# Kernel tuning notes

Hardware: AMD Instinct MI355X
Metric: run time of the kernel (lower is better)

Reference implementation:

```python
import jax, jax.numpy as jnp
import numpy as np

EMBED_DIM = 1024
NUM_HEADS = 16
HEAD_DIM = EMBED_DIM // NUM_HEADS


def setup_inputs() -> dict:
    key = jax.random.key(0)
    k_x, k_wqkv, k_bqkv, k_wo, k_bo = jax.random.split(key, 5)
    b, n = 2, 2048
    scale_in = 1.0 / np.sqrt(EMBED_DIM)
    return {
        "x": jax.random.normal(k_x, (b, n, EMBED_DIM), dtype=jnp.float32),
        "W_qkv": jax.random.normal(k_wqkv, (EMBED_DIM, 3 * EMBED_DIM), dtype=jnp.float32) * scale_in,
        "b_qkv": jnp.zeros((3 * EMBED_DIM,), dtype=jnp.float32),
        "W_out": jax.random.normal(k_wo, (EMBED_DIM, EMBED_DIM), dtype=jnp.float32) * scale_in,
        "b_out": jnp.zeros((EMBED_DIM,), dtype=jnp.float32),
    }


def _rope_rotate(t, cos, sin):
    # t: [b, h, n, hd]; cos/sin: [1, 1, n, hd//2]
    t1, t2 = jnp.split(t, 2, axis=-1)
    return jnp.concatenate([cos * t1 - sin * t2, sin * t1 + cos * t2], axis=-1)


def reference(x, W_qkv, b_qkv, W_out, b_out):
    b, n, d = x.shape
    h, hd = NUM_HEADS, HEAD_DIM

    qkv = x @ W_qkv + b_qkv                      # [b, n, 3d]
    q, k, v = jnp.split(qkv, 3, axis=-1)
    q, k, v = [t.reshape(b, n, h, hd).transpose(0, 2, 1, 3) for t in (q, k, v)]

    # RoPE tables
    hd2 = hd // 2
    theta = 10000.0 ** (-2.0 * jnp.arange(hd2, dtype=jnp.float32) / hd)
    freqs = jnp.arange(n, dtype=jnp.float32)[:, None] * theta[None, :]  # [n, hd2]
    cos = jnp.cos(freqs)[None, None]
    sin = jnp.sin(freqs)[None, None]
    q = _rope_rotate(q, cos, sin)
    k = _rope_rotate(k, cos, sin)

    scores = jnp.einsum('bhqd,bhkd->bhqk', q, k) / jnp.sqrt(jnp.float32(hd))
    attn = jax.nn.softmax(scores, axis=-1)       # [b, h, n, n]
    out = jnp.einsum('bhqk,bhkd->bhqd', attn, v)
    out = out.transpose(0, 2, 1, 3).reshape(b, n, d)
    return out @ W_out + b_out
```

## Files before the change

kernel.cpp:

```cpp
#include <hip/hip_runtime.h>
#include <hip/hip_bf16.h>
#include <math.h>

#define EMBED 1024
#define NHEAD 16
#define HD 64
#define BATCH 2
#define SEQ 2048
#define MTOT (BATCH * SEQ)
#define QKVN (3 * EMBED)

typedef __attribute__((ext_vector_type(8))) short short8;
typedef __attribute__((ext_vector_type(4))) float f32x4;

typedef __attribute__((address_space(1))) const unsigned int GUI;
typedef __attribute__((address_space(3))) unsigned int LUI;

__device__ __forceinline__ void gload_lds16(const void* src, void* dst) {
  __builtin_amdgcn_global_load_lds((GUI*)src, (LUI*)dst, 16, 0, 0);
}

__device__ __forceinline__ unsigned short f2bf(float f) {
  unsigned u = __builtin_bit_cast(unsigned, f);
  u += 0x7fffu + ((u >> 16) & 1u);
  return (unsigned short)(u >> 16);
}

__device__ __forceinline__ unsigned cvt_pk_bf16(float lo, float hi) {
  unsigned r;
  asm("v_cvt_pk_bf16_f32 %0, %1, %2" : "=v"(r) : "v"(lo), "v"(hi));
  return r;
}

#if __has_builtin(__builtin_amdgcn_exp2f)
#define EXP2(x) __builtin_amdgcn_exp2f(x)
#else
#define EXP2(x) __builtin_exp2f(x)
#endif

#define QSCALE 0.1803368801111191f


__global__ __launch_bounds__(256) void k_cvt(const float* __restrict__ in,
                                             unsigned short* __restrict__ out, int n4) {
  int i = blockIdx.x * 256 + threadIdx.x;
  if (i >= n4) return;
  float4 v = reinterpret_cast<const float4*>(in)[i];
  ushort4 o;
  o.x = f2bf(v.x); o.y = f2bf(v.y); o.z = f2bf(v.z); o.w = f2bf(v.w);
  reinterpret_cast<ushort4*>(out)[i] = o;
}

__global__ __launch_bounds__(256) void k_transpose_cvt(const float* __restrict__ W,
                                                       unsigned short* __restrict__ WT,
                                                       int K, int Ncols) {
  __shared__ float tile[32][33];
  int n0 = blockIdx.x * 32, k0 = blockIdx.y * 32;
  int tc = threadIdx.x & 31, tr = threadIdx.x >> 5;
  for (int i = 0; i < 4; i++) {
    int r = tr + i * 8;
    tile[r][tc] = W[(size_t)(k0 + r) * Ncols + n0 + tc];
  }
  __syncthreads();
  for (int i = 0; i < 4; i++) {
    int r = tr + i * 8;
    WT[(size_t)(n0 + r) * K + k0 + tc] = f2bf(tile[tc][r]);
  }
}

__global__ __launch_bounds__(256) void k_rope_tables(float* __restrict__ cosT,
                                                     float* __restrict__ sinT) {
  int idx = blockIdx.x * 256 + threadIdx.x;
  if (idx >= SEQ * 32) return;
  int pos = idx >> 5, i = idx & 31;
  float theta = __expf((float)i * -0.28782313662425575f);
  float f = (float)pos * theta;
  cosT[idx] = cosf(f);
  sinT[idx] = sinf(f);
}

__device__ __forceinline__ void gemm_mainloop(const unsigned short* __restrict__ A,
                                              const unsigned short* __restrict__ Bt,
                                              unsigned short* Al, unsigned short* Bl,
                                              size_t m0, size_t n0,
                                              int tid, int l15, int g, int wm, int wn,
                                              f32x4 acc[4][4]) {
  const int w = tid >> 6;
  const int lane = tid & 63;
  const int srow = lane >> 3, slot = lane & 7;
  for (int k0 = 0; k0 < 1024; k0 += 64) {
    __syncthreads();
    for (int it = 0; it < 4; it++) {
      const int r = w * 32 + it * 8 + srow;
      const int sc = (slot ^ (r & 7)) * 8;
      gload_lds16(A + (m0 + r) * 1024 + k0 + sc, &Al[(w * 32 + it * 8) * 64]);
      gload_lds16(Bt + (n0 + r) * 1024 + k0 + sc, &Bl[(w * 32 + it * 8) * 64]);
    }
    __syncthreads();
    for (int kk = 0; kk < 2; kk++) {
      short8 fa[4], fb[4];
      const int xr = ((kk * 4 + g) ^ (l15 & 7)) * 8;
      for (int i = 0; i < 4; i++)
        fa[i] = *reinterpret_cast<const short8*>(&Al[(wm * 64 + i * 16 + l15) * 64 + xr]);
      for (int j = 0; j < 4; j++)
        fb[j] = *reinterpret_cast<const short8*>(&Bl[(wn * 64 + j * 16 + l15) * 64 + xr]);
      for (int i = 0; i < 4; i++)
        for (int j = 0; j < 4; j++)
          acc[i][j] = __builtin_amdgcn_mfma_f32_16x16x32_bf16(fa[i], fb[j], acc[i][j], 0, 0, 0);
    }
  }
}

__global__ __launch_bounds__(256) void k_qkv_gemm(const unsigned short* __restrict__ A,
                                                  const unsigned short* __restrict__ Bt,
                                                  const float* __restrict__ bias,
                                                  const float* __restrict__ cosT,
                                                  const float* __restrict__ sinT,
                                                  unsigned short* __restrict__ Qb,
                                                  unsigned short* __restrict__ Kb,
                                                  unsigned short* __restrict__ Vtg) {
  __shared__ alignas(16) unsigned short Al[128 * 64];
  __shared__ alignas(16) unsigned short Bl[128 * 64];
  const int tid = threadIdx.x;
  const int lane = tid & 63, l15 = lane & 15, g = lane >> 4;
  const int wid = tid >> 6, wm = wid >> 1, wn = wid & 1;
  const int bid = blockIdx.x;
  const int tile = (bid & 7) * 96 + (bid >> 3);
  const size_t m0 = (size_t)(tile / 24) * 128;
  const size_t n0 = (size_t)(tile % 24) * 128;
  f32x4 acc[4][4] = {};
  gemm_mainloop(A, Bt, Al, Bl, m0, n0, tid, l15, g, wm, wn, acc);

  const int cbase = (int)n0 + wn * 64;
  const int sec = cbase >> 10;
  const int head = (cbase & 1023) >> 6;
  float bia[4];
  for (int j = 0; j < 4; j++) bia[j] = bias[cbase + j * 16 + l15];
  const size_t mw = m0 + wm * 64;

  if (sec == 2) {
    for (int i = 0; i < 4; i++) {
      size_t mbase = mw + i * 16 + g * 4;
      int bb = (int)(mbase >> 11), pos0 = (int)(mbase & 2047);
      int k0 = pos0 & 63;
      int col = (pos0 & ~63) | (k0 & 32) | (((k0 >> 2) & 3) << 3) | (((k0 >> 4) & 1) << 2);
      size_t hb = (size_t)(bb * NHEAD + head) * HD;
      for (int j = 0; j < 4; j++) {
        int d = j * 16 + l15;
        uint2 pk;
        pk.x = cvt_pk_bf16(acc[i][j][0] + bia[j], acc[i][j][1] + bia[j]);
        pk.y = cvt_pk_bf16(acc[i][j][2] + bia[j], acc[i][j][3] + bia[j]);
        *reinterpret_cast<uint2*>(Vtg + (hb + d) * SEQ + col) = pk;
      }
    }
  } else {
    unsigned short* dst = sec ? Kb : Qb;
    const float qs = sec ? 1.0f : QSCALE;
    for (int i = 0; i < 4; i++)
      for (int r = 0; r < 4; r++) {
        size_t m = mw + i * 16 + g * 4 + r;
        int bb = (int)(m >> 11), pos = (int)(m & 2047);
        size_t base = ((size_t)(bb * NHEAD + head) * SEQ + pos) * HD;
        const float* cr = cosT + pos * 32;
        const float* sr = sinT + pos * 32;
        for (int pl = 0; pl < 2; pl++) {
          int ii = pl * 16 + l15;
          float c = cr[ii], s = sr[ii];
          float lo = acc[i][pl][r] + bia[pl];
          float hi = acc[i][pl + 2][r] + bia[pl + 2];
          dst[base + ii]      = f2bf((c * lo - s * hi) * qs);
          dst[base + 32 + ii] = f2bf((s * lo + c * hi) * qs);
        }
      }
  }
}

__global__ __launch_bounds__(256) void k_out_gemm(const unsigned short* __restrict__ A,
                                                  const unsigned short* __restrict__ Bt,
                                                  const float* __restrict__ bias,
                                                  float* __restrict__ out) {
  __shared__ alignas(16) unsigned short Al[128 * 64];
  __shared__ alignas(16) unsigned short Bl[64 * 64];
  const int tid = threadIdx.x;
  const int lane = tid & 63, l15 = lane & 15, g = lane >> 4;
  const int wid = tid >> 6, wm = wid >> 1, wn = wid & 1;
  const int w = wid;
  const int srow = lane >> 3, slot = lane & 7;
  const int bid = blockIdx.x;
  const int tile = (bid & 7) * 64 + (bid >> 3);
  const size_t m0 = (size_t)(tile / 16) * 128;
  const size_t n0 = (size_t)(tile % 16) * 64;
  f32x4 acc[4][2] = {};

  for (int k0 = 0; k0 < 1024; k0 += 64) {
    __syncthreads();
    for (int it = 0; it < 4; it++) {
      const int r = w * 32 + it * 8 + srow;
      const int sc = (slot ^ (r & 7)) * 8;
      gload_lds16(A + (m0 + r) * 1024 + k0 + sc, &Al[(w * 32 + it * 8) * 64]);
    }
    for (int it = 0; it < 2; it++) {
      const int r = w * 16 + it * 8 + srow;
      const int sc = (slot ^ (r & 7)) * 8;
      gload_lds16(Bt + (n0 + r) * 1024 + k0 + sc, &Bl[(w * 16 + it * 8) * 64]);
    }
    __syncthreads();
    for (int kk = 0; kk < 2; kk++) {
      short8 fa[4], fb[2];
      const int xr = ((kk * 4 + g) ^ (l15 & 7)) * 8;
      for (int i = 0; i < 4; i++)
        fa[i] = *reinterpret_cast<const short8*>(&Al[(wm * 64 + i * 16 + l15) * 64 + xr]);
      for (int j = 0; j < 2; j++)
        fb[j] = *reinterpret_cast<const short8*>(&Bl[(wn * 32 + j * 16 + l15) * 64 + xr]);
      for (int i = 0; i < 4; i++)
        for (int j = 0; j < 2; j++)
          acc[i][j] = __builtin_amdgcn_mfma_f32_16x16x32_bf16(fa[i], fb[j], acc[i][j], 0, 0, 0);
    }
  }

  const int cbase = (int)n0 + wn * 32;
  const size_t mw = m0 + wm * 64;
  for (int i = 0; i < 4; i++)
    for (int r = 0; r < 4; r++) {
      size_t m = mw + i * 16 + g * 4 + r;
      for (int j = 0; j < 2; j++) {
        int col = cbase + j * 16 + l15;
        out[m * EMBED + col] = acc[i][j][r] + bias[col];
      }
    }
}

__global__ __launch_bounds__(256) void k_attn(const unsigned short* __restrict__ Q,
                                              const unsigned short* __restrict__ Kg,
                                              const unsigned short* __restrict__ Vtg,
                                              float* __restrict__ Opart,
                                              float* __restrict__ lpart) {
  __shared__ alignas(16) unsigned short Kt[2][64 * 64];
  __shared__ alignas(16) unsigned short Vt[2][64 * 64];
  const int tid = threadIdx.x, w = tid >> 6, lane = tid & 63;
  const int l15 = lane & 15, g = lane >> 4;
  const int srow = lane >> 3, slot = lane & 7;

  const int n = blockIdx.x;
  const int xcd = n & 7, m = n >> 3;
  const int qb = m & 15, z = m >> 4;
  const int sp = z & 1, bh = (z >> 1) * 8 + xcd;

  const unsigned short* Qp = Q + (size_t)bh * SEQ * HD;
  const unsigned short* Kp = Kg + (size_t)bh * SEQ * HD;
  const unsigned short* Vp = Vtg + (size_t)bh * HD * SEQ;
  const int q0 = qb * 128 + w * 32;

  short8 aq[2][2];
#pragma unroll
  for (int u = 0; u < 2; u++)
#pragma unroll
    for (int kk = 0; kk < 2; kk++)
      aq[u][kk] = *reinterpret_cast<const short8*>(
          Qp + (size_t)(q0 + u * 16 + l15) * HD + kk * 32 + g * 8);

  const int sr16 = w * 16 + srow;
  const int sc0 = (slot ^ (sr16 & 7)) * 8;
  const int kb0 = sp * 1024;

  const f32x4 z4 = {0.f, 0.f, 0.f, 0.f};
  f32x4 o[2][4] = {};
  float lrow[2] = {0.f, 0.f};

#define STAGE(tt, b)                                                             \
  do {                                                                           \
    const int kb_ = kb0 + (tt) * 64;                                             \
    gload_lds16(Kp + (size_t)(kb_ + sr16) * HD + sc0, &Kt[b][(w * 16) * 64]);    \
    gload_lds16(Vp + (size_t)sr16 * SEQ + kb_ + sc0, &Vt[b][(w * 16) * 64]);     \
    gload_lds16(Kp + (size_t)(kb_ + sr16 + 8) * HD + sc0,                        \
                &Kt[b][(w * 16 + 8) * 64]);                                      \
    gload_lds16(Vp + (size_t)(sr16 + 8) * SEQ + kb_ + sc0,                       \
                &Vt[b][(w * 16 + 8) * 64]);                                      \
  } while (0)

#define COMPUTE(cur)                                                             \
  do {                                                                           \
    const unsigned short* Ktc = Kt[cur];                                         \
    const unsigned short* Vtc = Vt[cur];                                         \
    f32x4 s[2][4];                                                               \
    {                                                                            \
      const int xr = (g ^ (l15 & 7)) * 8;                                        \
      _Pragma("unroll") for (int c = 0; c < 4; c++) {                            \
        short8 ak = *reinterpret_cast<const short8*>(&Ktc[(c * 16 + l15) * 64 + xr]); \
        s[0][c] = __builtin_amdgcn_mfma_f32_16x16x32_bf16(ak, aq[0][0], z4, 0, 0, 0); \
        s[1][c] = __builtin_amdgcn_mfma_f32_16x16x32_bf16(ak, aq[1][0], z4, 0, 0, 0); \
      }                                                                          \
    }                                                                            \
    {                                                                            \
      const int xr = ((4 + g) ^ (l15 & 7)) * 8;                                  \
      _Pragma("unroll") for (int c = 0; c < 4; c++) {                            \
        short8 ak = *reinterpret_cast<const short8*>(&Ktc[(c * 16 + l15) * 64 + xr]); \
        s[0][c] = __builtin_amdgcn_mfma_f32_16x16x32_bf16(ak, aq[0][1], s[0][c], 0, 0, 0); \
        s[1][c] = __builtin_amdgcn_mfma_f32_16x16x32_bf16(ak, aq[1][1], s[1][c], 0, 0, 0); \
      }                                                                          \
    }                                                                            \
    unsigned wpk[2][8];                                                          \
    _Pragma("unroll") for (int u = 0; u < 2; u++) {                              \
      float rs = 0.f;                                                            \
      _Pragma("unroll") for (int c = 0; c < 4; c++) {                            \
        float p0 = EXP2(s[u][c][0]);                                             \
        float p1 = EXP2(s[u][c][1]);                                             \
        float p2 = EXP2(s[u][c][2]);                                             \
        float p3 = EXP2(s[u][c][3]);                                             \
        rs += (p0 + p1) + (p2 + p3);                                             \
        wpk[u][2 * c]     = cvt_pk_bf16(p0, p1);                                 \
        wpk[u][2 * c + 1] = cvt_pk_bf16(p2, p3);                                 \
      }                                                                          \
      lrow[u] += rs;                                                             \
    }                                                                            \
    _Pragma("unroll") for (int kk = 0; kk < 2; kk++) {                           \
      const int xr = ((kk * 4 + g) ^ (l15 & 7)) * 8;                             \
      short8 pb0 = __builtin_bit_cast(short8,                                    \
          uint4{wpk[0][4 * kk], wpk[0][4 * kk + 1], wpk[0][4 * kk + 2], wpk[0][4 * kk + 3]}); \
      short8 pb1 = __builtin_bit_cast(short8,                                    \
          uint4{wpk[1][4 * kk], wpk[1][4 * kk + 1], wpk[1][4 * kk + 2], wpk[1][4 * kk + 3]}); \
      _Pragma("unroll") for (int c2 = 0; c2 < 4; c2++) {                         \
        short8 av = *reinterpret_cast<const short8*>(&Vtc[(c2 * 16 + l15) * 64 + xr]); \
        o[0][c2] = __builtin_amdgcn_mfma_f32_16x16x32_bf16(av, pb0, o[0][c2], 0, 0, 0); \
        o[1][c2] = __builtin_amdgcn_mfma_f32_16x16x32_bf16(av, pb1, o[1][c2], 0, 0, 0); \
      }                                                                          \
    }                                                                            \
  } while (0)

  STAGE(0, 0);

  for (int t = 0; t < 15; t++) {
    const int cur = t & 1;
    STAGE(t + 1, cur ^ 1);
    asm volatile("s_waitcnt vmcnt(4)" ::: "memory");
    __builtin_amdgcn_s_barrier();
    COMPUTE(cur);
    __builtin_amdgcn_s_barrier();
  }
  asm volatile("s_waitcnt vmcnt(0)" ::: "memory");
  __builtin_amdgcn_s_barrier();
  COMPUTE(1);

#undef STAGE
#undef COMPUTE

  const size_t ob = (size_t)(sp * 32 + bh) * SEQ * HD;
#pragma unroll
  for (int u = 0; u < 2; u++) {
    float l = lrow[u];
    l += __shfl_xor(l, 16, 64);
    l += __shfl_xor(l, 32, 64);
    const int pos = q0 + u * 16 + l15;
    if (g == 0) lpart[(size_t)(sp * 32 + bh) * SEQ + pos] = l;
    float* orow = Opart + ob + (size_t)pos * HD;
#pragma unroll
    for (int c2 = 0; c2 < 4; c2++)
      *reinterpret_cast<f32x4*>(orow + c2 * 16 + g * 4) = o[u][c2];
  }
}

__global__ __launch_bounds__(256) void k_merge(const float* __restrict__ Op,
                                               const float* __restrict__ lp,
                                               unsigned short* __restrict__ AO) {
  const int t = threadIdx.x;
  const int bh = blockIdx.x >> 5, pt = blockIdx.x & 31;
  const int pos = pt * 64 + (t >> 2), dc = (t & 3) * 16;
  const float* p0 = Op + ((size_t)bh * SEQ + pos) * HD + dc;
  const float* p1 = p0 + (size_t)32 * SEQ * HD;
  const float l = lp[(size_t)bh * SEQ + pos] + lp[(size_t)(32 + bh) * SEQ + pos];
  const float inv = 1.f / l;
  unsigned pk[8];
#pragma unroll
  for (int i = 0; i < 4; i++) {
    float4 a = reinterpret_cast<const float4*>(p0)[i];
    float4 b = reinterpret_cast<const float4*>(p1)[i];
    pk[2 * i]     = cvt_pk_bf16((a.x + b.x) * inv, (a.y + b.y) * inv);
    pk[2 * i + 1] = cvt_pk_bf16((a.z + b.z) * inv, (a.w + b.w) * inv);
  }
  const int bb = bh >> 4, h = bh & 15;
  unsigned short* dst = AO + ((size_t)bb * SEQ + pos) * EMBED + h * HD + dc;
  *reinterpret_cast<uint4*>(dst)     = uint4{pk[0], pk[1], pk[2], pk[3]};
  *reinterpret_cast<uint4*>(dst + 8) = uint4{pk[4], pk[5], pk[6], pk[7]};
}

extern "C" void kernel_launch(void* const* d_in, const int* in_sizes, int n_in,
                              void* d_out, int out_size, void* d_ws, size_t ws_size,
                              hipStream_t stream) {
  const float* x    = (const float*)d_in[0];
  const float* Wqkv = (const float*)d_in[1];
  const float* bqkv = (const float*)d_in[2];
  const float* Wout = (const float*)d_in[3];
  const float* bout = (const float*)d_in[4];
  float* out = (float*)d_out;

  char* ws = (char*)d_ws;
  size_t off = 0;
  auto carve = [&](size_t bytes) {
    char* p = ws + off;
    off += (bytes + 255) & ~(size_t)255;
    return p;
  };
  float* cosT           = (float*)carve((size_t)SEQ * 32 * 4);
  float* sinT           = (float*)carve((size_t)SEQ * 32 * 4);
  unsigned short* Xb    = (unsigned short*)carve((size_t)MTOT * EMBED * 2);
  unsigned short* WqkvT = (unsigned short*)carve((size_t)QKVN * EMBED * 2);
  unsigned short* WoT   = (unsigned short*)carve((size_t)EMBED * EMBED * 2);
  unsigned short* Qb    = (unsigned short*)carve((size_t)MTOT * EMBED * 2);
  unsigned short* Kb    = (unsigned short*)carve((size_t)MTOT * EMBED * 2);
  unsigned short* Vtg   = (unsigned short*)carve((size_t)MTOT * EMBED * 2);
  unsigned short* AO    = (unsigned short*)carve((size_t)MTOT * EMBED * 2);
  float* Opart          = (float*)carve((size_t)2 * 32 * HD * SEQ * 4);
  float* lpart          = (float*)carve((size_t)2 * 32 * SEQ * 4);

  k_cvt<<<(MTOT * EMBED / 4 + 255) / 256, 256, 0, stream>>>(x, Xb, MTOT * EMBED / 4);
  k_transpose_cvt<<<dim3(QKVN / 32, EMBED / 32), 256, 0, stream>>>(Wqkv, WqkvT, EMBED, QKVN);
  k_transpose_cvt<<<dim3(EMBED / 32, EMBED / 32), 256, 0, stream>>>(Wout, WoT, EMBED, EMBED);
  k_rope_tables<<<(SEQ * 32) / 256, 256, 0, stream>>>(cosT, sinT);

  k_qkv_gemm<<<dim3(768), 256, 0, stream>>>(Xb, WqkvT, bqkv, cosT, sinT, Qb, Kb, Vtg);
  k_attn<<<dim3(1024), 256, 0, stream>>>(Qb, Kb, Vtg, Opart, lpart);
  k_merge<<<dim3(1024), 256, 0, stream>>>(Opart, lpart, AO);
  k_out_gemm<<<dim3(512), 256, 0, stream>>>(AO, WoT, bout, out);
}
```

Baseline: 138.7 us.

## Double-buffer LDS in QKV and output GEMMs with K-step 32 prefetch

Replaces the single-buffered K=64 mainloop in both projection GEMMs with a double-buffered K=32 pipeline. The next stage's global-to-LDS loads are issued before computing the current one, with explicit vmcnt waits and barriers, so memory latency overlaps MFMA work. The LDS swizzle is changed to fit 32-wide rows. The cost is twice as many barrier pairs per K, less MFMA work per stage, and reliance on exact vmcnt counts for correctness.

Measured after the change: 155.1 us. +11.9%, slower.

```diff
diff --git a/kernel.cpp b/kernel.cpp
--- a/kernel.cpp
+++ b/kernel.cpp
@@ -79,38 +79,6 @@
   sinT[idx] = sinf(f);
 }
 
-__device__ __forceinline__ void gemm_mainloop(const unsigned short* __restrict__ A,
-                                              const unsigned short* __restrict__ Bt,
-                                              unsigned short* Al, unsigned short* Bl,
-                                              size_t m0, size_t n0,
-                                              int tid, int l15, int g, int wm, int wn,
-                                              f32x4 acc[4][4]) {
-  const int w = tid >> 6;
-  const int lane = tid & 63;
-  const int srow = lane >> 3, slot = lane & 7;
-  for (int k0 = 0; k0 < 1024; k0 += 64) {
-    __syncthreads();
-    for (int it = 0; it < 4; it++) {
-      const int r = w * 32 + it * 8 + srow;
-      const int sc = (slot ^ (r & 7)) * 8;
-      gload_lds16(A + (m0 + r) * 1024 + k0 + sc, &Al[(w * 32 + it * 8) * 64]);
-      gload_lds16(Bt + (n0 + r) * 1024 + k0 + sc, &Bl[(w * 32 + it * 8) * 64]);
-    }
-    __syncthreads();
-    for (int kk = 0; kk < 2; kk++) {
-      short8 fa[4], fb[4];
-      const int xr = ((kk * 4 + g) ^ (l15 & 7)) * 8;
-      for (int i = 0; i < 4; i++)
-        fa[i] = *reinterpret_cast<const short8*>(&Al[(wm * 64 + i * 16 + l15) * 64 + xr]);
-      for (int j = 0; j < 4; j++)
-        fb[j] = *reinterpret_cast<const short8*>(&Bl[(wn * 64 + j * 16 + l15) * 64 + xr]);
-      for (int i = 0; i < 4; i++)
-        for (int j = 0; j < 4; j++)
-          acc[i][j] = __builtin_amdgcn_mfma_f32_16x16x32_bf16(fa[i], fb[j], acc[i][j], 0, 0, 0);
-    }
-  }
-}
-
 __global__ __launch_bounds__(256) void k_qkv_gemm(const unsigned short* __restrict__ A,
                                                   const unsigned short* __restrict__ Bt,
                                                   const float* __restrict__ bias,
@@ -119,17 +87,62 @@
                                                   unsigned short* __restrict__ Qb,
                                                   unsigned short* __restrict__ Kb,
                                                   unsigned short* __restrict__ Vtg) {
-  __shared__ alignas(16) unsigned short Al[128 * 64];
-  __shared__ alignas(16) unsigned short Bl[128 * 64];
+  __shared__ alignas(16) unsigned short Al[2][128 * 32];
+  __shared__ alignas(16) unsigned short Bl[2][128 * 32];
   const int tid = threadIdx.x;
   const int lane = tid & 63, l15 = lane & 15, g = lane >> 4;
   const int wid = tid >> 6, wm = wid >> 1, wn = wid & 1;
+  const int w = wid;
+  const int lr = lane >> 2, slot = lane & 3;
+  const int schunk = slot ^ ((lr >> 2) & 3);
+  const int xrd = (l15 >> 2) & 3;
   const int bid = blockIdx.x;
   const int tile = (bid & 7) * 96 + (bid >> 3);
   const size_t m0 = (size_t)(tile / 24) * 128;
   const size_t n0 = (size_t)(tile % 24) * 128;
   f32x4 acc[4][4] = {};
-  gemm_mainloop(A, Bt, Al, Bl, m0, n0, tid, l15, g, wm, wn, acc);
+
+#define GSTAGE(k0_, b_)                                                          \
+  do {                                                                           \
+    _Pragma("unroll") for (int j = 0; j < 2; j++) {                              \
+      const int r = w * 32 + j * 16 + lr;                                        \
+      gload_lds16(A + (m0 + r) * 1024 + (k0_) + schunk * 8,                      \
+                  &Al[b_][(w * 32 + j * 16) * 32]);                              \
+      gload_lds16(Bt + (n0 + r) * 1024 + (k0_) + schunk * 8,                     \
+                  &Bl[b_][(w * 32 + j * 16) * 32]);                              \
+    }                                                                            \
+  } while (0)
+
+#define GCOMPUTE(cur)                                                            \
+  do {                                                                           \
+    short8 fa[4], fb[4];                                                         \
+    _Pragma("unroll") for (int i = 0; i < 4; i++)                                \
+      fa[i] = *reinterpret_cast<const short8*>(                                  \
+          &Al[cur][(wm * 64 + i * 16 + l15) * 32 + (g ^ xrd) * 8]);              \
+    _Pragma("unroll") for (int j = 0; j < 4; j++)                                \
+      fb[j] = *reinterpret_cast<const short8*>(                                  \
+          &Bl[cur][(wn * 64 + j * 16 + l15) * 32 + (g ^ xrd) * 8]);              \
+    _Pragma("unroll") for (int i = 0; i < 4; i++)                                \
+      _Pragma("unroll") for (int j = 0; j < 4; j++)                              \
+        acc[i][j] = __builtin_amdgcn_mfma_f32_16x16x32_bf16(fa[i], fb[j],        \
+                                                            acc[i][j], 0, 0, 0); \
+  } while (0)
+
+  GSTAGE(0, 0);
+  for (int t = 0; t < 31; t++) {
+    const int cur = t & 1;
+    GSTAGE((t + 1) * 32, cur ^ 1);
+    asm volatile("s_waitcnt vmcnt(4)" ::: "memory");
+    __builtin_amdgcn_s_barrier();
+    GCOMPUTE(cur);
+    __builtin_amdgcn_s_barrier();
+  }
+  asm volatile("s_waitcnt vmcnt(0)" ::: "memory");
+  __builtin_amdgcn_s_barrier();
+  GCOMPUTE(1);
+
+#undef GSTAGE
+#undef GCOMPUTE
 
   const int cbase = (int)n0 + wn * 64;
   const int sec = cbase >> 10;
@@ -179,44 +192,65 @@
                                                   const unsigned short* __restrict__ Bt,
                                                   const float* __restrict__ bias,
                                                   float* __restrict__ out) {
-  __shared__ alignas(16) unsigned short Al[128 * 64];
-  __shared__ alignas(16) unsigned short Bl[64 * 64];
+  __shared__ alignas(16) unsigned short Al[2][128 * 32];
+  __shared__ alignas(16) unsigned short Bl[2][64 * 32];
   const int tid = threadIdx.x;
   const int lane = tid & 63, l15 = lane & 15, g = lane >> 4;
   const int wid = tid >> 6, wm = wid >> 1, wn = wid & 1;
   const int w = wid;
-  const int srow = lane >> 3, slot = lane & 7;
+  const int lr = lane >> 2, slot = lane & 3;
+  const int schunk = slot ^ ((lr >> 2) & 3);
+  const int xrd = (l15 >> 2) & 3;
   const int bid = blockIdx.x;
   const int tile = (bid & 7) * 64 + (bid >> 3);
   const size_t m0 = (size_t)(tile / 16) * 128;
   const size_t n0 = (size_t)(tile % 16) * 64;
   f32x4 acc[4][2] = {};
 
-  for (int k0 = 0; k0 < 1024; k0 += 64) {
-    __syncthreads();
-    for (int it = 0; it < 4; it++) {
-      const int r = w * 32 + it * 8 + srow;
-      const int sc = (slot ^ (r & 7)) * 8;
-      gload_lds16(A + (m0 + r) * 1024 + k0 + sc, &Al[(w * 32 + it * 8) * 64]);
-    }
-    for (int it = 0; it < 2; it++) {
-      const int r = w * 16 + it * 8 + srow;
-      const int sc = (slot ^ (r & 7)) * 8;
-      gload_lds16(Bt + (n0 + r) * 1024 + k0 + sc, &Bl[(w * 16 + it * 8) * 64]);
-    }
-    __syncthreads();
-    for (int kk = 0; kk < 2; kk++) {
-      short8 fa[4], fb[2];
-      const int xr = ((kk * 4 + g) ^ (l15 & 7)) * 8;
-      for (int i = 0; i < 4; i++)
-        fa[i] = *reinterpret_cast<const short8*>(&Al[(wm * 64 + i * 16 + l15) * 64 + xr]);
-      for (int j = 0; j < 2; j++)
-        fb[j] = *reinterpret_cast<const short8*>(&Bl[(wn * 32 + j * 16 + l15) * 64 + xr]);
-      for (int i = 0; i < 4; i++)
-        for (int j = 0; j < 2; j++)
-          acc[i][j] = __builtin_amdgcn_mfma_f32_16x16x32_bf16(fa[i], fb[j], acc[i][j], 0, 0, 0);
-    }
-  }
+#define OSTAGE(k0_, b_)                                                          \
+  do {                                                                           \
+    _Pragma("unroll") for (int j = 0; j < 2; j++) {                              \
+      const int r = w * 32 + j * 16 + lr;                                        \
+      gload_lds16(A + (m0 + r) * 1024 + (k0_) + schunk * 8,                      \
+                  &Al[b_][(w * 32 + j * 16) * 32]);                              \
+    }                                                                            \
+    {                                                                            \
+      const int r = w * 16 + lr;                                                 \
+      gload_lds16(Bt + (n0 + r) * 1024 + (k0_) + schunk * 8,                     \
+                  &Bl[b_][(w * 16) * 32]);                                       \
+    }                                                                            \
+  } while (0)
+
+#define OCOMPUTE(cur)                                                            \
+  do {                                                                           \
+    short8 fa[4], fb[2];                                                         \
+    _Pragma("unroll") for (int i = 0; i < 4; i++)                                \
+      fa[i] = *reinterpret_cast<const short8*>(                                  \
+          &Al[cur][(wm * 64 + i * 16 + l15) * 32 + (g ^ xrd) * 8]);              \
+    _Pragma("unroll") for (int j = 0; j < 2; j++)                                \
+      fb[j] = *reinterpret_cast<const short8*>(                                  \
+          &Bl[cur][(wn * 32 + j * 16 + l15) * 32 + (g ^ xrd) * 8]);              \
+    _Pragma("unroll") for (int i = 0; i < 4; i++)                                \
+      _Pragma("unroll") for (int j = 0; j < 2; j++)                              \
+        acc[i][j] = __builtin_amdgcn_mfma_f32_16x16x32_bf16(fa[i], fb[j],        \
+                                                            acc[i][j], 0, 0, 0); \
+  } while (0)
+
+  OSTAGE(0, 0);
+  for (int t = 0; t < 31; t++) {
+    const int cur = t & 1;
+    OSTAGE((t + 1) * 32, cur ^ 1);
+    asm volatile("s_waitcnt vmcnt(3)" ::: "memory");
+    __builtin_amdgcn_s_barrier();
+    OCOMPUTE(cur);
+    __builtin_amdgcn_s_barrier();
+  }
+  asm volatile("s_waitcnt vmcnt(0)" ::: "memory");
+  __builtin_amdgcn_s_barrier();
+  OCOMPUTE(1);
+
+#undef OSTAGE
+#undef OCOMPUTE
 
   const int cbase = (int)n0 + wn * 32;
   const size_t mw = m0 + wm * 64;
```
